# Kernel tuning notes

Hardware: AMD Instinct MI355X
Metric: run time of the kernel (lower is better)

## Reference

```python
import jax, jax.numpy as jnp
import numpy as np

EMBED_DIM = 128
D3 = EMBED_DIM // 3  # 42
K = 3  # k = min(3, N-1); N >> 4 so k is statically 3


def _local_density(points):
    # points: [B, N, 3] -> mean distance to 3 nearest neighbors, [B, N, 1]
    sq = jnp.sum(points * points, axis=-1)  # [B, N]
    d2 = sq[:, :, None] + sq[:, None, :] - 2.0 * jnp.einsum('bnd,bmd->bnm', points, points)
    dists = jnp.sqrt(jnp.maximum(d2, 1e-12))  # [B, N, N]
    N = points.shape[1]
    eye = jnp.eye(N, dtype=bool)
    dists = jnp.where(eye[None, :, :], jnp.inf, dists)
    # k smallest = -(k largest of negated)
    neg_topk, _ = jax.lax.top_k(-dists, K)  # [B, N, K]
    return jnp.mean(-neg_topk, axis=-1, keepdims=True)  # [B, N, 1]


def setup_inputs() -> dict:
    key = jax.random.key(0)
    ks = jax.random.split(key, 9)
    B, N = 8, 4096
    points = jax.random.normal(ks[0], (B, N, 3), dtype=jnp.float32)
    # PyTorch Linear init scale: U(-1/sqrt(fan_in), 1/sqrt(fan_in))
    def lin(k, fan_in, fan_out):
        k1, k2 = jax.random.split(k)
        bnd = 1.0 / np.sqrt(fan_in)
        W = jax.random.uniform(k1, (fan_in, fan_out), jnp.float32, -bnd, bnd)
        b = jax.random.uniform(k2, (fan_out,), jnp.float32, -bnd, bnd)
        return W, b
    W_rel, b_rel = lin(ks[1], 3, D3)
    W_dist, b_dist = lin(ks[2], 1, D3)
    W_dens, b_dens = lin(ks[3], 1, D3)
    W_out, b_out = lin(ks[4], 3 * D3, EMBED_DIM)
    return {"points": points, "W_rel": W_rel, "b_rel": b_rel,
            "W_dist": W_dist, "b_dist": b_dist, "W_dens": W_dens, "b_dens": b_dens,
            "W_out": W_out, "b_out": b_out}


def reference(points, W_rel, b_rel, W_dist, b_dist, W_dens, b_dens, W_out, b_out):
    centroid = jnp.mean(points, axis=1, keepdims=True)          # [B, 1, 3]
    relative_pos = points - centroid                             # [B, N, 3]
    rel_features = relative_pos @ W_rel + b_rel                  # [B, N, D3]
    centroid_dist = jnp.linalg.norm(relative_pos, axis=-1, keepdims=True)  # [B, N, 1]
    dist_features = centroid_dist @ W_dist + b_dist              # [B, N, D3]
    local_density = _local_density(points)                       # [B, N, 1]
    density_features = local_density @ W_dens + b_dens           # [B, N, D3]
    features = jnp.concatenate([rel_features, dist_features, density_features], axis=-1)
    return features @ W_out + b_out                              # [B, N, 128]
```

## Files before the change

kernel.cpp:

```cpp
#include <hip/hip_runtime.h>
#include <math.h>

#define NPTS 4096
#define NBATCH 8

#define WS_CENT 0
#define WS_COEF 32

__launch_bounds__(256)
__global__ void prep_kernel(const float* __restrict__ pts,
                            const float* __restrict__ W_rel, const float* __restrict__ b_rel,
                            const float* __restrict__ W_dist, const float* __restrict__ b_dist,
                            const float* __restrict__ W_dens, const float* __restrict__ b_dens,
                            const float* __restrict__ W_out, const float* __restrict__ b_out,
                            float* __restrict__ ws) {
    __shared__ float sx[256], sy[256], sz[256];
    if (blockIdx.x < NBATCH) {
        int b = blockIdx.x;
        const float* P = pts + (size_t)b * NPTS * 3;
        float ax = 0.f, ay = 0.f, az = 0.f;
        for (int n = threadIdx.x; n < NPTS; n += 256) {
            ax += P[3 * n + 0];
            ay += P[3 * n + 1];
            az += P[3 * n + 2];
        }
        sx[threadIdx.x] = ax; sy[threadIdx.x] = ay; sz[threadIdx.x] = az;
        __syncthreads();
        for (int off = 128; off > 0; off >>= 1) {
            if (threadIdx.x < off) {
                sx[threadIdx.x] += sx[threadIdx.x + off];
                sy[threadIdx.x] += sy[threadIdx.x + off];
                sz[threadIdx.x] += sz[threadIdx.x + off];
            }
            __syncthreads();
        }
        if (threadIdx.x == 0) {
            const float inv = 1.0f / (float)NPTS;
            ws[WS_CENT + 4 * b + 0] = sx[0] * inv;
            ws[WS_CENT + 4 * b + 1] = sy[0] * inv;
            ws[WS_CENT + 4 * b + 2] = sz[0] * inv;
        }
    } else if (threadIdx.x < 128) {
        int o = threadIdx.x;
        float a0 = 0.f, a1 = 0.f, a2 = 0.f, vd = 0.f, vl = 0.f, be = b_out[o];
        for (int j = 0; j < 42; ++j) {
            float w0 = W_out[j * 128 + o];
            float w1 = W_out[(42 + j) * 128 + o];
            float w2 = W_out[(84 + j) * 128 + o];
            a0 = fmaf(W_rel[j],      w0, a0);
            a1 = fmaf(W_rel[42 + j], w0, a1);
            a2 = fmaf(W_rel[84 + j], w0, a2);
            vd = fmaf(W_dist[j],     w1, vd);
            vl = fmaf(W_dens[j],     w2, vl);
            be = fmaf(b_rel[j],  w0, be);
            be = fmaf(b_dist[j], w1, be);
            be = fmaf(b_dens[j], w2, be);
        }
        float* C = ws + WS_COEF;
        C[0 * 128 + o] = a0; C[1 * 128 + o] = a1; C[2 * 128 + o] = a2;
        C[3 * 128 + o] = vd; C[4 * 128 + o] = vl; C[5 * 128 + o] = be;
    }
}

#define INS3(t0, t1, t2, v)                                   \
    {                                                         \
        float n0 = fminf(t0, (v));                            \
        float n1 = __builtin_amdgcn_fmed3f(t0, t1, (v));      \
        float n2 = __builtin_amdgcn_fmed3f(t1, t2, (v));      \
        t0 = n0; t1 = n1; t2 = n2;                            \
    }

#define MERGE3(t0, t1, t2, m)                                 \
    {                                                         \
        float b0 = __shfl_xor(t0, m);                         \
        float b1 = __shfl_xor(t1, m);                         \
        float b2 = __shfl_xor(t2, m);                         \
        float X = fmaxf(t0, b0);                              \
        t0 = fminf(t0, b0);                                   \
        float Y = fminf(t1, b1);                              \
        float Z = fmaxf(X, Y);                                \
        t1 = fminf(X, Y);                                     \
        t2 = fminf(Z, fminf(t2, b2));                         \
    }

#define RFL(x) __uint_as_float(__builtin_amdgcn_readfirstlane(__float_as_uint(x)))

#define DECLQ(j)                                              \
    float4 Q##j = lp4[qb0 + ((j) ^ w)];                       \
    float qx##j = RFL(-2.0f * Q##j.x);                        \
    float qy##j = RFL(-2.0f * Q##j.y);                        \
    float qz##j = RFL(-2.0f * Q##j.z);                        \
    float sq##j = RFL(Q##j.w);                                \
    float t##j##0 = INFINITY, t##j##1 = INFINITY, t##j##2 = INFINITY;

#define STEP(j)                                                             \
    {                                                                       \
        float e = fmaf(qx##j, c.x, fmaf(qy##j, c.y, fmaf(qz##j, c.z, c.w)));\
        INS3(t##j##0, t##j##1, t##j##2, e);                                 \
    }

#define SELF(j)                                                             \
    if (lane == ((w << 3) + j)) {                                           \
        t##j##0 = t##j##1; t##j##1 = t##j##2; t##j##2 = INFINITY;           \
    }

#define MRG(j, m) MERGE3(t##j##0, t##j##1, t##j##2, m)

#define DENS(j)                                                             \
    float d##j = (sqrtf(fmaxf(t##j##0 + sq##j, 1e-12f)) +                   \
                  sqrtf(fmaxf(t##j##1 + sq##j, 1e-12f)) +                   \
                  sqrtf(fmaxf(t##j##2 + sq##j, 1e-12f))) * (1.0f / 3.0f);

__launch_bounds__(512, 4)
__global__ void density_out_kernel(const float* __restrict__ pts,
                                   const float* __restrict__ ws,
                                   float* __restrict__ out) {
    __shared__ float4 lp4[NPTS];
    __shared__ float dens[64];
    int b = blockIdx.x >> 6;
    int g = blockIdx.x & 63;
    int tid = threadIdx.x;
    int w = tid >> 6, lane = tid & 63;

    {
        const float4* P4 = (const float4*)(pts + (size_t)b * NPTS * 3);
        float4 v0 = P4[6 * tid + 0];
        float4 v1 = P4[6 * tid + 1];
        float4 v2 = P4[6 * tid + 2];
        float4 v3 = P4[6 * tid + 3];
        float4 v4 = P4[6 * tid + 4];
        float4 v5 = P4[6 * tid + 5];
        int mb = tid << 3;
        int sw = tid & 7;
        #define SQ4(x, y, z) make_float4((x), (y), (z), fmaf((x), (x), fmaf((y), (y), (z) * (z))))
        lp4[mb + (0 ^ sw)] = SQ4(v0.x, v0.y, v0.z);
        lp4[mb + (1 ^ sw)] = SQ4(v0.w, v1.x, v1.y);
        lp4[mb + (2 ^ sw)] = SQ4(v1.z, v1.w, v2.x);
        lp4[mb + (3 ^ sw)] = SQ4(v2.y, v2.z, v2.w);
        lp4[mb + (4 ^ sw)] = SQ4(v3.x, v3.y, v3.z);
        lp4[mb + (5 ^ sw)] = SQ4(v3.w, v4.x, v4.y);
        lp4[mb + (6 ^ sw)] = SQ4(v4.z, v4.w, v5.x);
        lp4[mb + (7 ^ sw)] = SQ4(v5.y, v5.z, v5.w);
        #undef SQ4
    }
    __syncthreads();

    int qb0 = (g << 6) + (w << 3);
    DECLQ(0) DECLQ(1) DECLQ(2) DECLQ(3) DECLQ(4) DECLQ(5) DECLQ(6) DECLQ(7)

    const float4* cbase = lp4 + (lane ^ ((lane >> 3) & 7));
    #pragma unroll 4
    for (int tile = 0; tile < 64; ++tile) {
        float4 c = cbase[tile << 6];
        STEP(0) STEP(1) STEP(2) STEP(3) STEP(4) STEP(5) STEP(6) STEP(7)
    }

    SELF(0) SELF(1) SELF(2) SELF(3) SELF(4) SELF(5) SELF(6) SELF(7)

    #pragma unroll
    for (int m = 1; m < 64; m <<= 1) {
        MRG(0, m) MRG(1, m) MRG(2, m) MRG(3, m)
        MRG(4, m) MRG(5, m) MRG(6, m) MRG(7, m)
    }

    DENS(0) DENS(1) DENS(2) DENS(3) DENS(4) DENS(5) DENS(6) DENS(7)
    if (lane == 0) {
        int db = w << 3;
        dens[db + 0] = d0; dens[db + 1] = d1; dens[db + 2] = d2; dens[db + 3] = d3;
        dens[db + 4] = d4; dens[db + 5] = d5; dens[db + 6] = d6; dens[db + 7] = d7;
    }
    __syncthreads();

    {
        int r = tid >> 3;
        int cb = (tid & 7) << 2;
        int m = (g << 6) + r;
        float4 p = lp4[m ^ ((m >> 3) & 7)];
        float cx = ws[WS_CENT + 4 * b + 0];
        float cy = ws[WS_CENT + 4 * b + 1];
        float cz = ws[WS_CENT + 4 * b + 2];
        float rx = p.x - cx, ry = p.y - cy, rz = p.z - cz;
        float cd = sqrtf(fmaf(rx, rx, fmaf(ry, ry, rz * rz)));
        float ld = dens[r];
        const float4* Cg = (const float4*)(ws + WS_COEF);
        float4* orow = (float4*)(out + ((size_t)b * NPTS + m) * 128);
        #pragma unroll
        for (int h = 0; h < 4; ++h) {
            int ob = cb + h;
            float4 A0 = Cg[0 * 32 + ob];
            float4 A1 = Cg[1 * 32 + ob];
            float4 A2 = Cg[2 * 32 + ob];
            float4 VD = Cg[3 * 32 + ob];
            float4 VL = Cg[4 * 32 + ob];
            float4 BE = Cg[5 * 32 + ob];
            float4 rv;
            rv.x = fmaf(rx, A0.x, fmaf(ry, A1.x, fmaf(rz, A2.x, fmaf(cd, VD.x, fmaf(ld, VL.x, BE.x)))));
            rv.y = fmaf(rx, A0.y, fmaf(ry, A1.y, fmaf(rz, A2.y, fmaf(cd, VD.y, fmaf(ld, VL.y, BE.y)))));
            rv.z = fmaf(rx, A0.z, fmaf(ry, A1.z, fmaf(rz, A2.z, fmaf(cd, VD.z, fmaf(ld, VL.z, BE.z)))));
            rv.w = fmaf(rx, A0.w, fmaf(ry, A1.w, fmaf(rz, A2.w, fmaf(cd, VD.w, fmaf(ld, VL.w, BE.w)))));
            orow[ob] = rv;
        }
    }
}

extern "C" void kernel_launch(void* const* d_in, const int* in_sizes, int n_in,
                              void* d_out, int out_size, void* d_ws, size_t ws_size,
                              hipStream_t stream) {
    const float* pts    = (const float*)d_in[0];
    const float* W_rel  = (const float*)d_in[1];
    const float* b_rel  = (const float*)d_in[2];
    const float* W_dist = (const float*)d_in[3];
    const float* b_dist = (const float*)d_in[4];
    const float* W_dens = (const float*)d_in[5];
    const float* b_dens = (const float*)d_in[6];
    const float* W_out  = (const float*)d_in[7];
    const float* b_out  = (const float*)d_in[8];
    float* out = (float*)d_out;
    float* ws  = (float*)d_ws;

    hipLaunchKernelGGL(prep_kernel, dim3(NBATCH + 1), dim3(256), 0, stream,
                       pts, W_rel, b_rel, W_dist, b_dist, W_dens, b_dens, W_out, b_out, ws);
    hipLaunchKernelGGL(density_out_kernel, dim3(NBATCH * 64), dim3(512), 0, stream,
                       pts, ws, out);
}
```

Measured before the change: 43.63 us.

## Split density scan into half-candidate blocks and separate output kernel

The fused density+output kernel becomes two kernels. A scan kernel assigns each query group two blocks that each scan half of the candidate points (32KB LDS instead of 64KB, launch bounds raised to 8 blocks/CU), writing partial top-3 lists to workspace. A separate output kernel merges the two partial lists, computes density and writes the 128-wide output rows. This doubles the grid and raises occupancy to better fill the CUs, at the cost of an extra launch and workspace round trip.

Result: slower. 59.15 us (+35.6%).

```diff
diff --git a/kernel.cpp b/kernel.cpp
--- a/kernel.cpp
+++ b/kernel.cpp
@@ -6,6 +6,7 @@
 
 #define WS_CENT 0
 #define WS_COEF 32
+#define WS_TRI  1024
 
 __launch_bounds__(256)
 __global__ void prep_kernel(const float* __restrict__ pts,
@@ -85,12 +86,15 @@
 
 #define RFL(x) __uint_as_float(__builtin_amdgcn_readfirstlane(__float_as_uint(x)))
 
-#define DECLQ(j)                                              \
-    float4 Q##j = lp4[qb0 + ((j) ^ w)];                       \
-    float qx##j = RFL(-2.0f * Q##j.x);                        \
-    float qy##j = RFL(-2.0f * Q##j.y);                        \
-    float qz##j = RFL(-2.0f * Q##j.z);                        \
-    float sq##j = RFL(Q##j.w);                                \
+#define SIG(m) ((m) ^ (((m) >> 3) & 7))
+
+#define DECLQ(j)                                                          \
+    float xq##j = QP[3 * (j) + 0];                                        \
+    float yq##j = QP[3 * (j) + 1];                                        \
+    float zq##j = QP[3 * (j) + 2];                                        \
+    float qx##j = RFL(-2.0f * xq##j);                                     \
+    float qy##j = RFL(-2.0f * yq##j);                                     \
+    float qz##j = RFL(-2.0f * zq##j);                                     \
     float t##j##0 = INFINITY, t##j##1 = INFINITY, t##j##2 = INFINITY;
 
 #define STEP(j)                                                             \
@@ -100,61 +104,50 @@
     }
 
 #define SELF(j)                                                             \
-    if (lane == ((w << 3) + j)) {                                           \
+    if (selfhalf && lane == ((w << 3) + (j))) {                             \
         t##j##0 = t##j##1; t##j##1 = t##j##2; t##j##2 = INFINITY;           \
     }
 
 #define MRG(j, m) MERGE3(t##j##0, t##j##1, t##j##2, m)
 
-#define DENS(j)                                                             \
-    float d##j = (sqrtf(fmaxf(t##j##0 + sq##j, 1e-12f)) +                   \
-                  sqrtf(fmaxf(t##j##1 + sq##j, 1e-12f)) +                   \
-                  sqrtf(fmaxf(t##j##2 + sq##j, 1e-12f))) * (1.0f / 3.0f);
-
-__launch_bounds__(512, 4)
-__global__ void density_out_kernel(const float* __restrict__ pts,
-                                   const float* __restrict__ ws,
-                                   float* __restrict__ out) {
-    __shared__ float4 lp4[NPTS];
-    __shared__ float dens[64];
-    int b = blockIdx.x >> 6;
-    int g = blockIdx.x & 63;
+__launch_bounds__(512, 8)
+__global__ void scan_kernel(const float* __restrict__ pts, float* __restrict__ ws) {
+    __shared__ float4 lp4[2048];
+    int blk = blockIdx.x;
+    int b  = blk >> 7;
+    int h  = (blk >> 6) & 1;
+    int qg = blk & 63;
     int tid = threadIdx.x;
     int w = tid >> 6, lane = tid & 63;
 
     {
-        const float4* P4 = (const float4*)(pts + (size_t)b * NPTS * 3);
-        float4 v0 = P4[6 * tid + 0];
-        float4 v1 = P4[6 * tid + 1];
-        float4 v2 = P4[6 * tid + 2];
-        float4 v3 = P4[6 * tid + 3];
-        float4 v4 = P4[6 * tid + 4];
-        float4 v5 = P4[6 * tid + 5];
-        int mb = tid << 3;
-        int sw = tid & 7;
+        const float4* P4 = (const float4*)(pts + ((size_t)b * NPTS + (size_t)h * 2048) * 3);
+        float4 v0 = P4[3 * tid + 0];
+        float4 v1 = P4[3 * tid + 1];
+        float4 v2 = P4[3 * tid + 2];
+        int mb = tid << 2;
         #define SQ4(x, y, z) make_float4((x), (y), (z), fmaf((x), (x), fmaf((y), (y), (z) * (z))))
-        lp4[mb + (0 ^ sw)] = SQ4(v0.x, v0.y, v0.z);
-        lp4[mb + (1 ^ sw)] = SQ4(v0.w, v1.x, v1.y);
-        lp4[mb + (2 ^ sw)] = SQ4(v1.z, v1.w, v2.x);
-        lp4[mb + (3 ^ sw)] = SQ4(v2.y, v2.z, v2.w);
-        lp4[mb + (4 ^ sw)] = SQ4(v3.x, v3.y, v3.z);
-        lp4[mb + (5 ^ sw)] = SQ4(v3.w, v4.x, v4.y);
-        lp4[mb + (6 ^ sw)] = SQ4(v4.z, v4.w, v5.x);
-        lp4[mb + (7 ^ sw)] = SQ4(v5.y, v5.z, v5.w);
+        lp4[SIG(mb + 0)] = SQ4(v0.x, v0.y, v0.z);
+        lp4[SIG(mb + 1)] = SQ4(v0.w, v1.x, v1.y);
+        lp4[SIG(mb + 2)] = SQ4(v1.z, v1.w, v2.x);
+        lp4[SIG(mb + 3)] = SQ4(v2.y, v2.z, v2.w);
         #undef SQ4
     }
+
+    int nq = (qg << 6) + (w << 3);
+    const float* QP = pts + ((size_t)b * NPTS + nq) * 3;
+    DECLQ(0) DECLQ(1) DECLQ(2) DECLQ(3) DECLQ(4) DECLQ(5) DECLQ(6) DECLQ(7)
+
     __syncthreads();
 
-    int qb0 = (g << 6) + (w << 3);
-    DECLQ(0) DECLQ(1) DECLQ(2) DECLQ(3) DECLQ(4) DECLQ(5) DECLQ(6) DECLQ(7)
-
-    const float4* cbase = lp4 + (lane ^ ((lane >> 3) & 7));
+    const float4* cbase = lp4 + SIG(lane);
     #pragma unroll 4
-    for (int tile = 0; tile < 64; ++tile) {
+    for (int tile = 0; tile < 32; ++tile) {
         float4 c = cbase[tile << 6];
         STEP(0) STEP(1) STEP(2) STEP(3) STEP(4) STEP(5) STEP(6) STEP(7)
     }
 
+    bool selfhalf = (h == (qg >> 5));
     SELF(0) SELF(1) SELF(2) SELF(3) SELF(4) SELF(5) SELF(6) SELF(7)
 
     #pragma unroll
@@ -163,43 +156,65 @@
         MRG(4, m) MRG(5, m) MRG(6, m) MRG(7, m)
     }
 
-    DENS(0) DENS(1) DENS(2) DENS(3) DENS(4) DENS(5) DENS(6) DENS(7)
     if (lane == 0) {
-        int db = w << 3;
-        dens[db + 0] = d0; dens[db + 1] = d1; dens[db + 2] = d2; dens[db + 3] = d3;
-        dens[db + 4] = d4; dens[db + 5] = d5; dens[db + 6] = d6; dens[db + 7] = d7;
-    }
-    __syncthreads();
-
-    {
-        int r = tid >> 3;
-        int cb = (tid & 7) << 2;
-        int m = (g << 6) + r;
-        float4 p = lp4[m ^ ((m >> 3) & 7)];
-        float cx = ws[WS_CENT + 4 * b + 0];
-        float cy = ws[WS_CENT + 4 * b + 1];
-        float cz = ws[WS_CENT + 4 * b + 2];
-        float rx = p.x - cx, ry = p.y - cy, rz = p.z - cz;
-        float cd = sqrtf(fmaf(rx, rx, fmaf(ry, ry, rz * rz)));
-        float ld = dens[r];
-        const float4* Cg = (const float4*)(ws + WS_COEF);
-        float4* orow = (float4*)(out + ((size_t)b * NPTS + m) * 128);
-        #pragma unroll
-        for (int h = 0; h < 4; ++h) {
-            int ob = cb + h;
-            float4 A0 = Cg[0 * 32 + ob];
-            float4 A1 = Cg[1 * 32 + ob];
-            float4 A2 = Cg[2 * 32 + ob];
-            float4 VD = Cg[3 * 32 + ob];
-            float4 VL = Cg[4 * 32 + ob];
-            float4 BE = Cg[5 * 32 + ob];
-            float4 rv;
-            rv.x = fmaf(rx, A0.x, fmaf(ry, A1.x, fmaf(rz, A2.x, fmaf(cd, VD.x, fmaf(ld, VL.x, BE.x)))));
-            rv.y = fmaf(rx, A0.y, fmaf(ry, A1.y, fmaf(rz, A2.y, fmaf(cd, VD.y, fmaf(ld, VL.y, BE.y)))));
-            rv.z = fmaf(rx, A0.z, fmaf(ry, A1.z, fmaf(rz, A2.z, fmaf(cd, VD.z, fmaf(ld, VL.z, BE.z)))));
-            rv.w = fmaf(rx, A0.w, fmaf(ry, A1.w, fmaf(rz, A2.w, fmaf(cd, VD.w, fmaf(ld, VL.w, BE.w)))));
-            orow[ob] = rv;
-        }
+        float4* T = (float4*)(ws + WS_TRI) + ((((size_t)b * NPTS + nq) << 1) + h);
+        T[0]  = make_float4(t00, t01, t02, 0.f);
+        T[2]  = make_float4(t10, t11, t12, 0.f);
+        T[4]  = make_float4(t20, t21, t22, 0.f);
+        T[6]  = make_float4(t30, t31, t32, 0.f);
+        T[8]  = make_float4(t40, t41, t42, 0.f);
+        T[10] = make_float4(t50, t51, t52, 0.f);
+        T[12] = make_float4(t60, t61, t62, 0.f);
+        T[14] = make_float4(t70, t71, t72, 0.f);
+    }
+}
+
+__launch_bounds__(256)
+__global__ void output_kernel(const float* __restrict__ pts, const float* __restrict__ ws,
+                              float* __restrict__ out) {
+    int row = blockIdx.x * 16 + (threadIdx.x >> 4);
+    int b = row >> 12;
+    int c16 = threadIdx.x & 15;
+
+    const float4* T = (const float4*)(ws + WS_TRI) + ((size_t)row << 1);
+    float4 ta = T[0], tb = T[1];
+    float X  = fmaxf(ta.x, tb.x);
+    float m0 = fminf(ta.x, tb.x);
+    float Y  = fminf(ta.y, tb.y);
+    float m1 = fminf(X, Y);
+    float Z  = fmaxf(X, Y);
+    float m2 = fminf(Z, fminf(ta.z, tb.z));
+
+    const float* P = pts + (size_t)row * 3;
+    float px = P[0], py = P[1], pz = P[2];
+    float sq = fmaf(px, px, fmaf(py, py, pz * pz));
+    float ld = (sqrtf(fmaxf(m0 + sq, 1e-12f)) +
+                sqrtf(fmaxf(m1 + sq, 1e-12f)) +
+                sqrtf(fmaxf(m2 + sq, 1e-12f))) * (1.0f / 3.0f);
+
+    float cx = ws[WS_CENT + 4 * b + 0];
+    float cy = ws[WS_CENT + 4 * b + 1];
+    float cz = ws[WS_CENT + 4 * b + 2];
+    float rx = px - cx, ry = py - cy, rz = pz - cz;
+    float cd = sqrtf(fmaf(rx, rx, fmaf(ry, ry, rz * rz)));
+
+    const float4* Cg = (const float4*)(ws + WS_COEF);
+    float4* orow = (float4*)(out + (size_t)row * 128);
+    #pragma unroll
+    for (int hh = 0; hh < 2; ++hh) {
+        int ob = (c16 << 1) + hh;
+        float4 A0 = Cg[0 * 32 + ob];
+        float4 A1 = Cg[1 * 32 + ob];
+        float4 A2 = Cg[2 * 32 + ob];
+        float4 VD = Cg[3 * 32 + ob];
+        float4 VL = Cg[4 * 32 + ob];
+        float4 BE = Cg[5 * 32 + ob];
+        float4 rv;
+        rv.x = fmaf(rx, A0.x, fmaf(ry, A1.x, fmaf(rz, A2.x, fmaf(cd, VD.x, fmaf(ld, VL.x, BE.x)))));
+        rv.y = fmaf(rx, A0.y, fmaf(ry, A1.y, fmaf(rz, A2.y, fmaf(cd, VD.y, fmaf(ld, VL.y, BE.y)))));
+        rv.z = fmaf(rx, A0.z, fmaf(ry, A1.z, fmaf(rz, A2.z, fmaf(cd, VD.z, fmaf(ld, VL.z, BE.z)))));
+        rv.w = fmaf(rx, A0.w, fmaf(ry, A1.w, fmaf(rz, A2.w, fmaf(cd, VD.w, fmaf(ld, VL.w, BE.w)))));
+        orow[ob] = rv;
     }
 }
 
@@ -220,6 +235,6 @@
 
     hipLaunchKernelGGL(prep_kernel, dim3(NBATCH + 1), dim3(256), 0, stream,
                        pts, W_rel, b_rel, W_dist, b_dist, W_dens, b_dens, W_out, b_out, ws);
-    hipLaunchKernelGGL(density_out_kernel, dim3(NBATCH * 64), dim3(512), 0, stream,
-                       pts, ws, out);
-}
+    hipLaunchKernelGGL(scan_kernel, dim3(1024), dim3(512), 0, stream, pts, ws);
+    hipLaunchKernelGGL(output_kernel, dim3(2048), dim3(256), 0, stream, pts, ws, out);
+}
```
